# Kernel tuning notes

Measured on AMD Instinct MI355X. Metric: run time of the kernel, lower is better.

## Reference

```python
import jax, jax.numpy as jnp
import numpy as np

V_MIN = -10.0
V_MAX = 10.0
NUM_ATOMS = 251
B = 131072
N_OBS = 128
N_ACT = 32
HID = 512


def _ln(x, g, b, eps=1e-5):
    m = jnp.mean(x, axis=-1, keepdims=True)
    v = jnp.var(x, axis=-1, keepdims=True)
    return (x - m) * jax.lax.rsqrt(v + eps) * g + b


def setup_inputs() -> dict:
    key = jax.random.key(0)
    ks = jax.random.split(key, 16)

    def lin(k, fi, fo):
        kw, kb = jax.random.split(k)
        lim = 1.0 / np.sqrt(fi)
        W = jax.random.uniform(kw, (fi, fo), jnp.float32, -lim, lim)
        b = jax.random.uniform(kb, (fo,), jnp.float32, -lim, lim)
        return W, b

    W1, b1 = lin(ks[0], N_OBS + N_ACT, HID)
    W2, b2 = lin(ks[1], HID, HID // 2)
    W3, b3 = lin(ks[2], HID // 2, HID // 4)
    W4, b4 = lin(ks[3], HID // 4, NUM_ATOMS)

    return {
        "obs": jax.random.normal(ks[4], (B, N_OBS), jnp.float32),
        "actions": jax.random.normal(ks[5], (B, N_ACT), jnp.float32),
        "rewards": jax.random.normal(ks[6], (B,), jnp.float32),
        "bootstrap": (jax.random.uniform(ks[7], (B,)) > 0.05).astype(jnp.float32),
        "discount": jnp.full((B,), 0.99, jnp.float32),
        "q_support": jnp.linspace(V_MIN, V_MAX, NUM_ATOMS, dtype=jnp.float32),
        "W1": W1, "b1": b1, "g1": jnp.ones((HID,), jnp.float32), "be1": jnp.zeros((HID,), jnp.float32),
        "W2": W2, "b2": b2, "g2": jnp.ones((HID // 2,), jnp.float32), "be2": jnp.zeros((HID // 2,), jnp.float32),
        "W3": W3, "b3": b3, "g3": jnp.ones((HID // 4,), jnp.float32), "be3": jnp.zeros((HID // 4,), jnp.float32),
        "W4": W4, "b4": b4,
    }


def _net(obs, actions, W1, b1, g1, be1, W2, b2, g2, be2, W3, b3, g3, be3, W4, b4):
    x = jnp.concatenate([obs, actions], axis=1)
    x = jax.nn.silu(_ln(x @ W1 + b1, g1, be1))
    x = jax.nn.silu(_ln(x @ W2 + b2, g2, be2))
    x = jax.nn.silu(_ln(x @ W3 + b3, g3, be3))
    return x @ W4 + b4  # [B, NUM_ATOMS] logits


def reference(obs, actions, rewards, bootstrap, discount, q_support,
              W1, b1, g1, be1, W2, b2, g2, be2, W3, b3, g3, be3, W4, b4):
    # C51 categorical projection (DistributionalQNetwork.projection)
    delta_z = (V_MAX - V_MIN) / (NUM_ATOMS - 1)
    bsz = rewards.shape[0]
    target_z = rewards[:, None] + bootstrap[:, None] * discount[:, None] * q_support[None, :]
    target_z = jnp.clip(target_z, V_MIN, V_MAX)
    b = (target_z - V_MIN) / delta_z  # fractional bin positions [B, A]
    lower = jnp.floor(b).astype(jnp.int32)
    upper = jnp.ceil(b).astype(jnp.int32)
    is_integer = upper == lower
    lower_mask = (lower > 0) & is_integer
    upper_mask = (lower == 0) & is_integer
    lower = jnp.where(lower_mask, lower - 1, lower)
    upper = jnp.where(upper_mask, upper + 1, upper)

    logits = _net(obs, actions, W1, b1, g1, be1, W2, b2, g2, be2, W3, b3, g3, be3, W4, b4)
    next_dist = jax.nn.softmax(logits, axis=1)

    offset = (jnp.arange(bsz, dtype=jnp.int32) * NUM_ATOMS)[:, None]  # [B,1]
    max_index = bsz * NUM_ATOMS - 1
    li = jnp.clip((lower + offset).reshape(-1), 0, max_index)
    ui = jnp.clip((upper + offset).reshape(-1), 0, max_index)

    w_lo = (next_dist * (upper.astype(jnp.float32) - b)).reshape(-1)
    w_hi = (next_dist * (b - lower.astype(jnp.float32))).reshape(-1)

    proj = jnp.zeros((bsz * NUM_ATOMS,), next_dist.dtype)
    proj = proj.at[li].add(w_lo).at[ui].add(w_hi)
    return proj.reshape(bsz, NUM_ATOMS)
```

## Files before the change

kernel.cpp:

```cpp
#include <hip/hip_runtime.h>


#define THREADS 256
#define PREP_THREADS 256

typedef __attribute__((ext_vector_type(8))) short short8v;
typedef __attribute__((ext_vector_type(4))) float f32x4;

__device__ __forceinline__ unsigned short f2bf(float f) {
  union { float f; unsigned u; } v; v.f = f;
  unsigned u = v.u;
  u += 0x7fffu + ((u >> 16) & 1u);
  return (unsigned short)(u >> 16);
}
__device__ __forceinline__ unsigned pack2bf(float a, float b) {
  return (unsigned)f2bf(a) | ((unsigned)f2bf(b) << 16);
}

__global__ void prep_kernel(const float* __restrict__ W1, const float* __restrict__ W2,
                            const float* __restrict__ W3, const float* __restrict__ W4,
                            unsigned short* __restrict__ ws) {
  int i = blockIdx.x * PREP_THREADS + threadIdx.x;
  if (i < 81920) {
    int n = i / 160, k = i - n * 160;
    ws[i] = f2bf(W1[k * 512 + n]);
  } else if (i < 212992) {
    int j = i - 81920; int n = j >> 9, k = j & 511;
    ws[i] = f2bf(W2[k * 256 + n]);
  } else if (i < 245760) {
    int j = i - 212992; int n = j >> 8, k = j & 255;
    ws[i] = f2bf(W3[k * 128 + n]);
  } else if (i < 278528) {
    int j = i - 245760; int n = j >> 7, k = j & 127;
    ws[i] = (n < 251) ? f2bf(W4[k * 251 + n]) : (unsigned short)0;
  }
}

#define OFF_A   0
#define OFF_B   32768
#define OFF_ZS  49152
#define OFF_B4  50176
#define OFF_RED 51200
#define LDS_TOTAL 52480

template<int KD, int NFT>
__device__ __forceinline__ void gemm_w(const unsigned short* __restrict__ WT,
                                       const unsigned char* __restrict__ Hb,
                                       int fbase, f32x4 (&acc)[NFT][2]) {
  const int lane = threadIdx.x & 63;
  const int lm = lane & 15, kg = lane >> 4;
  int woff[NFT];
#pragma unroll
  for (int ft = 0; ft < NFT; ++ft)
    woff[ft] = (fbase + ft * 16 + lm) * KD + kg * 8;
  const unsigned char* bp[2][2];
#pragma unroll
  for (int rt = 0; rt < 2; ++rt) {
    const int r = rt * 16 + lm;
    const int swz = (r & 7) << 4;
    const int base = r * (KD * 2) + kg * 16;
    bp[rt][0] = Hb + ((base) ^ swz);
    bp[rt][1] = Hb + ((base + 64) ^ swz);
  }
#pragma unroll
  for (int ks = 0; ks < KD / 32; ++ks) {
    const int koff = (ks >> 1) * 128;
    const short8v b0 = *(const short8v*)(bp[0][ks & 1] + koff);
    const short8v b1 = *(const short8v*)(bp[1][ks & 1] + koff);
#pragma unroll
    for (int ft = 0; ft < NFT; ++ft) {
      const short8v a = *(const short8v*)(WT + woff[ft] + ks * 32);
      acc[ft][0] = __builtin_amdgcn_mfma_f32_16x16x32_bf16(a, b0, acc[ft][0], 0, 0, 0);
      acc[ft][1] = __builtin_amdgcn_mfma_f32_16x16x32_bf16(a, b1, acc[ft][1], 0, 0, 0);
    }
  }
}

template<int ND, int NFT>
__device__ __forceinline__ void ln_silu_store(
    f32x4 (&acc)[NFT][2],
    const float* __restrict__ bias, const float* __restrict__ g,
    const float* __restrict__ be, unsigned char* __restrict__ Hb,
    float* __restrict__ redL, int fbase, int fq)
{
  const int lane = threadIdx.x & 63;
  const int lm = lane & 15, kg = lane >> 4;
  float s[2] = {0.f, 0.f}, q[2] = {0.f, 0.f};
#pragma unroll
  for (int ft = 0; ft < NFT; ++ft) {
    const int f0 = fbase + ft * 16 + kg * 4;
    const f32x4 bb = *(const f32x4*)(bias + f0);
#pragma unroll
    for (int rt = 0; rt < 2; ++rt)
#pragma unroll
      for (int rg = 0; rg < 4; ++rg) {
        float x = acc[ft][rt][rg] + bb[rg];
        acc[ft][rt][rg] = x;
        s[rt] += x; q[rt] += x * x;
      }
  }
#pragma unroll
  for (int rt = 0; rt < 2; ++rt) {
    s[rt] += __shfl_xor(s[rt], 16); s[rt] += __shfl_xor(s[rt], 32);
    q[rt] += __shfl_xor(q[rt], 16); q[rt] += __shfl_xor(q[rt], 32);
  }
  if (lane < 16) {
#pragma unroll
    for (int rt = 0; rt < 2; ++rt) {
      redL[(rt * 16 + lm) * 9 + fq * 2    ] = s[rt];
      redL[(rt * 16 + lm) * 9 + fq * 2 + 1] = q[rt];
    }
  }
  __syncthreads();
  float mean[2], rstd[2];
#pragma unroll
  for (int rt = 0; rt < 2; ++rt) {
    const int row = rt * 16 + lm;
    float S = 0.f, Q = 0.f;
#pragma unroll
    for (int w = 0; w < 4; ++w) {
      S += redL[row * 9 + w * 2];
      Q += redL[row * 9 + w * 2 + 1];
    }
    float m = S * (1.0f / ND);
    float v = Q * (1.0f / ND) - m * m;
    mean[rt] = m; rstd[rt] = rsqrtf(v + 1e-5f);
  }
#pragma unroll
  for (int ft = 0; ft < NFT; ++ft) {
    const int f0 = fbase + ft * 16 + kg * 4;
    const f32x4 g4 = *(const f32x4*)(g + f0);
    const f32x4 e4 = *(const f32x4*)(be + f0);
#pragma unroll
    for (int rt = 0; rt < 2; ++rt) {
      const int row = rt * 16 + lm;
      float h[4];
#pragma unroll
      for (int rg = 0; rg < 4; ++rg) {
        float y = (acc[ft][rt][rg] - mean[rt]) * rstd[rt] * g4[rg] + e4[rg];
        h[rg] = y * (1.0f / (1.0f + __expf(-y)));
      }
      uint2 w; w.x = pack2bf(h[0], h[1]); w.y = pack2bf(h[2], h[3]);
      int byte = row * (ND * 2) + f0 * 2;
      byte ^= ((row & 7) << 4);
      *(uint2*)(Hb + byte) = w;
    }
  }
}

__global__ __launch_bounds__(THREADS, 3) void fused_kernel(
    const float* __restrict__ obs, const float* __restrict__ actions,
    const float* __restrict__ rewards, const float* __restrict__ bootstrap,
    const float* __restrict__ discount, const float* __restrict__ q_support,
    const float* __restrict__ b1, const float* __restrict__ g1, const float* __restrict__ be1,
    const float* __restrict__ b2, const float* __restrict__ g2, const float* __restrict__ be2,
    const float* __restrict__ b3, const float* __restrict__ g3, const float* __restrict__ be3,
    const float* __restrict__ b4,
    const unsigned short* __restrict__ ws,
    float* __restrict__ out)
{
  __shared__ __align__(16) unsigned char smem[LDS_TOTAL];
  const int tid  = threadIdx.x;
  const int fq   = tid >> 6;
  const int lane = tid & 63;
  const int lm   = lane & 15;
  const int kg   = lane >> 4;
  const int row0 = blockIdx.x * 32;

  const unsigned short* W1T = ws;
  const unsigned short* W2T = ws + 81920;
  const unsigned short* W3T = ws + 212992;
  const unsigned short* W4T = ws + 245760;

  float* zsL  = (float*)(smem + OFF_ZS);
  float* b4L  = (float*)(smem + OFF_B4);
  float* redL = (float*)(smem + OFF_RED);

  float rw[2], bt[2], dc[2];
#pragma unroll
  for (int rt = 0; rt < 2; ++rt) {
    const int r = row0 + rt * 16 + lm;
    rw[rt] = rewards[r]; bt[rt] = bootstrap[r]; dc[rt] = discount[r];
  }

  zsL[tid] = (tid < 251) ? q_support[tid] : 0.f;
  b4L[tid] = (tid < 251) ? b4[tid] : 0.f;

  {
    unsigned char* Xb = smem + OFF_B;
#pragma unroll
    for (int it = 0; it < 5; ++it) {
      const int qq = it * THREADS + tid;
      const int r  = qq / 40;
      const int c4 = (qq - r * 40) * 4;
      float4 v;
      if (c4 < 128) v = *(const float4*)(obs + (size_t)(row0 + r) * 128 + c4);
      else          v = *(const float4*)(actions + (size_t)(row0 + r) * 32 + (c4 - 128));
      uint2 w; w.x = pack2bf(v.x, v.y); w.y = pack2bf(v.z, v.w);
      int byte = r * 320 + c4 * 2;
      byte ^= ((r & 7) << 4);
      *(uint2*)(Xb + byte) = w;
    }
  }
  __syncthreads();

  f32x4 acc1[8][2];
#pragma unroll
  for (int i = 0; i < 8; ++i) { acc1[i][0] = f32x4{0,0,0,0}; acc1[i][1] = f32x4{0,0,0,0}; }
  gemm_w<160, 8>(W1T, smem + OFF_B, fq * 128, acc1);
  ln_silu_store<512, 8>(acc1, b1, g1, be1, smem + OFF_A, redL, fq * 128, fq);
  __syncthreads();

  f32x4 acc2[4][2];
#pragma unroll
  for (int i = 0; i < 4; ++i) { acc2[i][0] = f32x4{0,0,0,0}; acc2[i][1] = f32x4{0,0,0,0}; }
  gemm_w<512, 4>(W2T, smem + OFF_A, fq * 64, acc2);
  ln_silu_store<256, 4>(acc2, b2, g2, be2, smem + OFF_B, redL, fq * 64, fq);
  __syncthreads();

  f32x4 acc3[2][2];
#pragma unroll
  for (int i = 0; i < 2; ++i) { acc3[i][0] = f32x4{0,0,0,0}; acc3[i][1] = f32x4{0,0,0,0}; }
  gemm_w<256, 2>(W3T, smem + OFF_B, fq * 32, acc3);
  ln_silu_store<128, 2>(acc3, b3, g3, be3, smem + OFF_A, redL, fq * 32, fq);
  __syncthreads();

  f32x4 acc4[4][2];
#pragma unroll
  for (int i = 0; i < 4; ++i) { acc4[i][0] = f32x4{0,0,0,0}; acc4[i][1] = f32x4{0,0,0,0}; }
  gemm_w<128, 4>(W4T, smem + OFF_A, fq * 64, acc4);

  float lv[4][2][4];
#pragma unroll
  for (int ft = 0; ft < 4; ++ft) {
    const int f0 = fq * 64 + ft * 16 + kg * 4;
    const f32x4 bb = *(const f32x4*)(b4L + f0);
#pragma unroll
    for (int rt = 0; rt < 2; ++rt)
#pragma unroll
      for (int rg = 0; rg < 4; ++rg) {
        const int f = f0 + rg;
        lv[ft][rt][rg] = (f < 251) ? (acc4[ft][rt][rg] + bb[rg]) : -1e30f;
      }
  }

#pragma unroll
  for (int rt = 0; rt < 2; ++rt) {
    float m = lv[0][rt][0];
#pragma unroll
    for (int ft = 0; ft < 4; ++ft)
#pragma unroll
      for (int rg = 0; rg < 4; ++rg) m = fmaxf(m, lv[ft][rt][rg]);
    m = fmaxf(m, __shfl_xor(m, 16));
    m = fmaxf(m, __shfl_xor(m, 32));
    if (lane < 16) redL[(rt * 16 + lm) * 5 + fq] = m;
  }
  __syncthreads();

  float* projL = (float*)(smem + OFF_A);
  for (int i = tid; i < 32 * 251; i += THREADS) projL[i] = 0.f;

  float gm[2];
#pragma unroll
  for (int rt = 0; rt < 2; ++rt) {
    const int row = rt * 16 + lm;
    float m = redL[row * 5];
#pragma unroll
    for (int w = 1; w < 4; ++w) m = fmaxf(m, redL[row * 5 + w]);
    gm[rt] = m;
  }
  __syncthreads();
#pragma unroll
  for (int rt = 0; rt < 2; ++rt) {
    float E = 0.f;
#pragma unroll
    for (int ft = 0; ft < 4; ++ft)
#pragma unroll
      for (int rg = 0; rg < 4; ++rg) {
        float e = __expf(lv[ft][rt][rg] - gm[rt]);
        lv[ft][rt][rg] = e;
        E += e;
      }
    E += __shfl_xor(E, 16); E += __shfl_xor(E, 32);
    if (lane < 16) redL[(rt * 16 + lm) * 5 + fq] = E;
  }
  __syncthreads();
  float inv[2];
#pragma unroll
  for (int rt = 0; rt < 2; ++rt) {
    const int row = rt * 16 + lm;
    float E = 0.f;
#pragma unroll
    for (int w = 0; w < 4; ++w) E += redL[row * 5 + w];
    inv[rt] = 1.0f / E;
  }

  constexpr float DZF = 20.0f / 250.0f;
#pragma unroll
  for (int ft = 0; ft < 4; ++ft) {
    const int f0 = fq * 64 + ft * 16 + kg * 4;
    const f32x4 z4 = *(const f32x4*)(zsL + f0);
#pragma unroll
    for (int rt = 0; rt < 2; ++rt) {
      const int base = (rt * 16 + lm) * 251;
      const float bd = __fmul_rn(bt[rt], dc[rt]);
#pragma unroll
      for (int rg = 0; rg < 4; ++rg) {
        const int f = f0 + rg;
        if (f < 251) {
          const float p = lv[ft][rt][rg] * inv[rt];
          float t = __fadd_rn(rw[rt], __fmul_rn(bd, z4[rg]));
          t = fminf(fmaxf(t, -10.0f), 10.0f);
          const float bfr = __fdiv_rn(__fsub_rn(t, -10.0f), DZF);
          const float fl = floorf(bfr), fu = ceilf(bfr);
          int l = (int)fl, u = (int)fu;
          if (fl == fu) { if (l > 0) --l; else ++u; }
          atomicAdd(projL + base + l, p * ((float)u - bfr));
          atomicAdd(projL + base + u, p * (bfr - (float)l));
        }
      }
    }
  }
  __syncthreads();

  const float4* ps = (const float4*)projL;
  float4* po = (float4*)(out + (size_t)row0 * 251);
  for (int i = tid; i < 2008; i += THREADS) po[i] = ps[i];
}

extern "C" void kernel_launch(void* const* d_in, const int* in_sizes, int n_in,
                              void* d_out, int out_size, void* d_ws, size_t ws_size,
                              hipStream_t stream) {
  const float* obs  = (const float*)d_in[0];
  const float* act  = (const float*)d_in[1];
  const float* rew  = (const float*)d_in[2];
  const float* boot = (const float*)d_in[3];
  const float* disc = (const float*)d_in[4];
  const float* zs   = (const float*)d_in[5];
  const float* W1   = (const float*)d_in[6];
  const float* b1   = (const float*)d_in[7];
  const float* g1   = (const float*)d_in[8];
  const float* be1  = (const float*)d_in[9];
  const float* W2   = (const float*)d_in[10];
  const float* b2   = (const float*)d_in[11];
  const float* g2   = (const float*)d_in[12];
  const float* be2  = (const float*)d_in[13];
  const float* W3   = (const float*)d_in[14];
  const float* b3   = (const float*)d_in[15];
  const float* g3   = (const float*)d_in[16];
  const float* be3  = (const float*)d_in[17];
  const float* W4   = (const float*)d_in[18];
  const float* b4   = (const float*)d_in[19];
  unsigned short* wsp = (unsigned short*)d_ws;

  const int Bn = in_sizes[2];
  prep_kernel<<<(278528 + PREP_THREADS - 1) / PREP_THREADS, PREP_THREADS, 0, stream>>>(
      W1, W2, W3, W4, wsp);
  fused_kernel<<<Bn / 32, THREADS, 0, stream>>>(obs, act, rew, boot, disc, zs,
      b1, g1, be1, b2, g2, be2, b3, g3, be3, b4, wsp, (float*)d_out);
}
```

Baseline: 508.0 us.

## Alias activation LDS buffers in place and double-buffer GEMM operand loads

The two ping-pong LDS activation regions are merged into one region that each layer overwrites in place, cutting shared memory per block. Launch bounds rise from 3 to 4 blocks per CU so more waves can be resident. The weight-stationary GEMM now prefetches the next k-step's weight and activation fragments into registers while the current MFMAs run. The tighter register budget from the higher launch bound, together with the extra prefetch buffers, risks spills. In-place reuse also depends on the layer-norm routine synchronizing all waves before any of them writes.

```diff
diff --git a/kernel.cpp b/kernel.cpp
--- a/kernel.cpp
+++ b/kernel.cpp
@@ -36,12 +36,11 @@
   }
 }
 
-#define OFF_A   0
-#define OFF_B   32768
-#define OFF_ZS  49152
-#define OFF_B4  50176
-#define OFF_RED 51200
-#define LDS_TOTAL 52480
+#define OFF_R   0
+#define OFF_ZS  32768
+#define OFF_B4  33792
+#define OFF_RED 34816
+#define LDS_TOTAL 36096
 
 template<int KD, int NFT>
 __device__ __forceinline__ void gemm_w(const unsigned short* __restrict__ WT,
@@ -49,29 +48,57 @@
                                        int fbase, f32x4 (&acc)[NFT][2]) {
   const int lane = threadIdx.x & 63;
   const int lm = lane & 15, kg = lane >> 4;
+  constexpr int KS  = KD / 32;
+  constexpr int G   = (NFT > 4) ? 2 : 1;
+  constexpr int FPG = NFT / G;
+  constexpr int NIT = KS * G;
+
   int woff[NFT];
 #pragma unroll
   for (int ft = 0; ft < NFT; ++ft)
     woff[ft] = (fbase + ft * 16 + lm) * KD + kg * 8;
-  const unsigned char* bp[2][2];
+
+  int boff[2][2];
 #pragma unroll
   for (int rt = 0; rt < 2; ++rt) {
     const int r = rt * 16 + lm;
     const int swz = (r & 7) << 4;
     const int base = r * (KD * 2) + kg * 16;
-    bp[rt][0] = Hb + ((base) ^ swz);
-    bp[rt][1] = Hb + ((base + 64) ^ swz);
-  }
-#pragma unroll
-  for (int ks = 0; ks < KD / 32; ++ks) {
-    const int koff = (ks >> 1) * 128;
-    const short8v b0 = *(const short8v*)(bp[0][ks & 1] + koff);
-    const short8v b1 = *(const short8v*)(bp[1][ks & 1] + koff);
-#pragma unroll
-    for (int ft = 0; ft < NFT; ++ft) {
-      const short8v a = *(const short8v*)(WT + woff[ft] + ks * 32);
-      acc[ft][0] = __builtin_amdgcn_mfma_f32_16x16x32_bf16(a, b0, acc[ft][0], 0, 0, 0);
-      acc[ft][1] = __builtin_amdgcn_mfma_f32_16x16x32_bf16(a, b1, acc[ft][1], 0, 0, 0);
+    boff[rt][0] = base ^ swz;
+    boff[rt][1] = (base + 64) ^ swz;
+  }
+
+  short8v abuf[2][FPG];
+  short8v bbuf[2][2];
+#pragma unroll
+  for (int rt = 0; rt < 2; ++rt)
+    bbuf[0][rt] = *(const short8v*)(Hb + boff[rt][0]);
+#pragma unroll
+  for (int f = 0; f < FPG; ++f)
+    abuf[0][f] = *(const short8v*)(WT + woff[f]);
+
+#pragma unroll
+  for (int it = 0; it < NIT; ++it) {
+    const int ks = it / G, g = it % G;
+    const int cur = it & 1, nxt = cur ^ 1;
+    if (it + 1 < NIT) {
+      const int nit = it + 1;
+      const int nks = nit / G, ng = nit % G;
+      if (ng == 0) {
+        const int koff = (nks >> 1) * 128;
+#pragma unroll
+        for (int rt = 0; rt < 2; ++rt)
+          bbuf[nks & 1][rt] = *(const short8v*)(Hb + boff[rt][nks & 1] + koff);
+      }
+#pragma unroll
+      for (int f = 0; f < FPG; ++f)
+        abuf[nxt][f] = *(const short8v*)(WT + woff[ng * FPG + f] + nks * 32);
+    }
+#pragma unroll
+    for (int f = 0; f < FPG; ++f) {
+      const int ft = g * FPG + f;
+      acc[ft][0] = __builtin_amdgcn_mfma_f32_16x16x32_bf16(abuf[cur][f], bbuf[ks & 1][0], acc[ft][0], 0, 0, 0);
+      acc[ft][1] = __builtin_amdgcn_mfma_f32_16x16x32_bf16(abuf[cur][f], bbuf[ks & 1][1], acc[ft][1], 0, 0, 0);
     }
   }
 }
@@ -148,7 +175,7 @@
   }
 }
 
-__global__ __launch_bounds__(THREADS, 3) void fused_kernel(
+__global__ __launch_bounds__(THREADS, 4) void fused_kernel(
     const float* __restrict__ obs, const float* __restrict__ actions,
     const float* __restrict__ rewards, const float* __restrict__ bootstrap,
     const float* __restrict__ discount, const float* __restrict__ q_support,
@@ -187,7 +214,7 @@
   b4L[tid] = (tid < 251) ? b4[tid] : 0.f;
 
   {
-    unsigned char* Xb = smem + OFF_B;
+    unsigned char* Xb = smem + OFF_R;
 #pragma unroll
     for (int it = 0; it < 5; ++it) {
       const int qq = it * THREADS + tid;
@@ -207,28 +234,28 @@
   f32x4 acc1[8][2];
 #pragma unroll
   for (int i = 0; i < 8; ++i) { acc1[i][0] = f32x4{0,0,0,0}; acc1[i][1] = f32x4{0,0,0,0}; }
-  gemm_w<160, 8>(W1T, smem + OFF_B, fq * 128, acc1);
-  ln_silu_store<512, 8>(acc1, b1, g1, be1, smem + OFF_A, redL, fq * 128, fq);
+  gemm_w<160, 8>(W1T, smem + OFF_R, fq * 128, acc1);
+  ln_silu_store<512, 8>(acc1, b1, g1, be1, smem + OFF_R, redL, fq * 128, fq);
   __syncthreads();
 
   f32x4 acc2[4][2];
 #pragma unroll
   for (int i = 0; i < 4; ++i) { acc2[i][0] = f32x4{0,0,0,0}; acc2[i][1] = f32x4{0,0,0,0}; }
-  gemm_w<512, 4>(W2T, smem + OFF_A, fq * 64, acc2);
-  ln_silu_store<256, 4>(acc2, b2, g2, be2, smem + OFF_B, redL, fq * 64, fq);
+  gemm_w<512, 4>(W2T, smem + OFF_R, fq * 64, acc2);
+  ln_silu_store<256, 4>(acc2, b2, g2, be2, smem + OFF_R, redL, fq * 64, fq);
   __syncthreads();
 
   f32x4 acc3[2][2];
 #pragma unroll
   for (int i = 0; i < 2; ++i) { acc3[i][0] = f32x4{0,0,0,0}; acc3[i][1] = f32x4{0,0,0,0}; }
-  gemm_w<256, 2>(W3T, smem + OFF_B, fq * 32, acc3);
-  ln_silu_store<128, 2>(acc3, b3, g3, be3, smem + OFF_A, redL, fq * 32, fq);
+  gemm_w<256, 2>(W3T, smem + OFF_R, fq * 32, acc3);
+  ln_silu_store<128, 2>(acc3, b3, g3, be3, smem + OFF_R, redL, fq * 32, fq);
   __syncthreads();
 
   f32x4 acc4[4][2];
 #pragma unroll
   for (int i = 0; i < 4; ++i) { acc4[i][0] = f32x4{0,0,0,0}; acc4[i][1] = f32x4{0,0,0,0}; }
-  gemm_w<128, 4>(W4T, smem + OFF_A, fq * 64, acc4);
+  gemm_w<128, 4>(W4T, smem + OFF_R, fq * 64, acc4);
 
   float lv[4][2][4];
 #pragma unroll
@@ -257,7 +284,7 @@
   }
   __syncthreads();
 
-  float* projL = (float*)(smem + OFF_A);
+  float* projL = (float*)(smem + OFF_R);
   for (int i = tid; i < 32 * 251; i += THREADS) projL[i] = 0.f;
 
   float gm[2];
```

Result: faster. 482.8 us (-4.9%).
